# Kernel tuning notes

Hardware: AMD Instinct MI355X
Metric: run time of the kernel (lower is better)

Reference implementation:

```python
import jax, jax.numpy as jnp
import numpy as np

EMBED_DIM = 2048
NUM_HEADS = 16
HEAD_DIM = EMBED_DIM // NUM_HEADS
BATCH, SEQ = 4, 4096


def setup_inputs() -> dict:
    key = jax.random.key(0)
    k1, k2, k3, k4 = jax.random.split(key, 4)
    scale = 1.0 / np.sqrt(EMBED_DIM)
    x = jax.random.normal(k1, (BATCH, SEQ, EMBED_DIM), dtype=jnp.float32)
    W_qkv = jax.random.normal(k2, (EMBED_DIM, 3 * EMBED_DIM), dtype=jnp.float32) * scale
    W_out = jax.random.normal(k3, (EMBED_DIM, EMBED_DIM), dtype=jnp.float32) * scale
    b_out = jax.random.normal(k4, (EMBED_DIM,), dtype=jnp.float32) * 0.01
    return {"x": x, "W_qkv": W_qkv, "W_out": W_out, "b_out": b_out}


def reference(x, W_qkv, W_out, b_out):
    b, s, _ = x.shape
    # qkv: (b, s, 3, h, d)
    qkv = (x @ W_qkv).reshape(b, s, 3, NUM_HEADS, HEAD_DIM)
    q, k, v = qkv[:, :, 0], qkv[:, :, 1], qkv[:, :, 2]
    # NOTE: faithful to source — scores mix HEADS per token: (b, s, h, h)
    scores = jnp.einsum('bshd,bsHd->bshH', q, k) / jnp.sqrt(jnp.float32(HEAD_DIM))
    w = jax.nn.softmax(scores, axis=-1)
    attn = jnp.einsum('bshH,bsHd->bshd', w, v).reshape(b, s, EMBED_DIM)
    return attn @ W_out + b_out
```

## Files before the change

kernel.cpp:

```cpp
#include <hip/hip_runtime.h>
#include <hip/hip_bf16.h>
#include <cstdint>


#define TOKENS 16384
#define EMB    2048
#define NQKV   6144

typedef __bf16 bf16x8_t __attribute__((ext_vector_type(8)));
typedef float  f32x4_t  __attribute__((ext_vector_type(4)));

#define GLOAD16(gsrc, ldst)                                                    \
  __builtin_amdgcn_global_load_lds(                                            \
      (const __attribute__((address_space(1))) void*)(uintptr_t)(gsrc),        \
      (__attribute__((address_space(3))) void*)(uint32_t)(uintptr_t)(ldst),    \
      16, 0, 0)

static __device__ __forceinline__ unsigned short f32_to_bf16_bits(float f) {
  union { float f; uint32_t u; } x; x.f = f;
  uint32_t u = x.u;
  u += 0x7fffu + ((u >> 16) & 1u);
  return (unsigned short)(u >> 16);
}

__global__ __launch_bounds__(256) void cvt_f32_bf16(
    const float4* __restrict__ in, ushort4* __restrict__ out, int n4) {
  const int stride = gridDim.x * blockDim.x;
  for (int i = blockIdx.x * blockDim.x + threadIdx.x; i < n4; i += stride) {
    float4 v = in[i];
    ushort4 o;
    o.x = f32_to_bf16_bits(v.x);
    o.y = f32_to_bf16_bits(v.y);
    o.z = f32_to_bf16_bits(v.z);
    o.w = f32_to_bf16_bits(v.w);
    out[i] = o;
  }
}

__global__ __launch_bounds__(256) void transpose_cvt(
    const float* __restrict__ in, unsigned short* __restrict__ out, int R, int C) {
  __shared__ float tile[32][33];
  const int bx = blockIdx.x * 32;
  const int by = blockIdx.y * 32;
  const int tx = threadIdx.x;
  const int ty = threadIdx.y;
#pragma unroll
  for (int j = 0; j < 32; j += 8)
    tile[ty + j][tx] = in[(size_t)(by + ty + j) * C + bx + tx];
  __syncthreads();
#pragma unroll
  for (int j = 0; j < 32; j += 8)
    out[(size_t)(bx + ty + j) * R + by + tx] = f32_to_bf16_bits(tile[tx][ty + j]);
}

template <bool OUT_BF16>
__global__ __launch_bounds__(512, 1) void gemm_bt(
    const unsigned short* __restrict__ A,
    const unsigned short* __restrict__ BT,
    unsigned short* __restrict__ Cb,
    float* __restrict__ Cf,
    const float* __restrict__ bias,
    int M, int N) {
  constexpr int K = 2048;
  constexpr int BK = 64;
  constexpr int NKT = K / BK;
  __shared__ __align__(16) char lds[131072];

  const int nbx = N / 256;
  const int nwg = gridDim.x;
  const int bid = blockIdx.x;
  const int swzb = (bid & 7) * (nwg >> 3) + (bid >> 3);
  const int by = swzb / nbx;
  const int bx = swzb % nbx;

  const int t    = threadIdx.x;
  const int lane = t & 63;
  const int wid  = t >> 6;
  const int wr   = wid >> 2;
  const int wc   = wid & 3;
  const int lr   = lane & 15;
  const int g    = lane >> 4;

  const unsigned short* aSrc = A  + (size_t)by * 256 * K;
  const unsigned short* bSrc = BT + (size_t)bx * 256 * K;

  int aoff[2], boff[2];
#pragma unroll
  for (int i = 0; i < 2; ++i) {
    const int p   = (i * 512 + t) * 16;
    const int lo  = p ^ (((p >> 7) & 7) << 4);
    const int rih = lo >> 7;
    const int kbe = (lo & 127) >> 1;
    aoff[i] = (((rih >> 6) << 7) + (rih & 63)) * K + kbe;
    boff[i] = (((rih >> 5) << 6) + (rih & 31)) * K + kbe;
  }
  const int ldst = wid << 10;

  auto stageA = [&](int h, int k0, char* bufA) {
#pragma unroll
    for (int i = 0; i < 2; ++i)
      GLOAD16(aSrc + aoff[i] + h * (64 * K) + k0, bufA + h * 16384 + i * 8192 + ldst);
  };
  auto stageB = [&](int h, int k0, char* bufB) {
#pragma unroll
    for (int i = 0; i < 2; ++i)
      GLOAD16(bSrc + boff[i] + h * (32 * K) + k0, bufB + h * 16384 + i * 8192 + ldst);
  };

  const int sw   = (lr & 7) << 4;
  const int col0 = (g * 16) ^ sw;
  const int col1 = (64 + g * 16) ^ sw;
  const int aRow = (wr * 64 + lr) * 128;
  const int bRow = (wc * 32 + lr) * 128;

  f32x4_t acc[8][4] = {};
  bf16x8_t av[4][2];
  bf16x8_t bvA[2][2], bvB[2][2];
  bf16x8_t bv1[2][2];

#define LDA_INTO(dst, bufA_, q)                                                \
  {                                                                            \
    const char* _b = (bufA_) + (q) * 16384 + aRow;                             \
    _Pragma("unroll") for (int m2 = 0; m2 < 4; ++m2) {                         \
      dst[m2][0] = *(const bf16x8_t*)(_b + m2 * 2048 + col0);                  \
      dst[m2][1] = *(const bf16x8_t*)(_b + m2 * 2048 + col1);                  \
    }                                                                          \
  }
#define LDB_INTO(dst, bufB_, pair)                                             \
  {                                                                            \
    _Pragma("unroll") for (int e = 0; e < 2; ++e) {                            \
      const int nf = (pair) * 2 + e;                                           \
      const char* _b = (bufB_) + (nf >> 1) * 16384 + (nf & 1) * 2048 + bRow;   \
      dst[e][0] = *(const bf16x8_t*)(_b + col0);                               \
      dst[e][1] = *(const bf16x8_t*)(_b + col1);                               \
    }                                                                          \
  }
#define MFMAQ(AV, BV, Q, PAIR)                                                 \
  _Pragma("unroll") for (int m2 = 0; m2 < 4; ++m2)                             \
  _Pragma("unroll") for (int e = 0; e < 2; ++e)                                \
  _Pragma("unroll") for (int ks = 0; ks < 2; ++ks)                             \
    acc[(Q) * 4 + m2][(PAIR) * 2 + e] = __builtin_amdgcn_mfma_f32_16x16x32_bf16( \
        AV[m2][ks], BV[e][ks], acc[(Q) * 4 + m2][(PAIR) * 2 + e], 0, 0, 0);

#define SBR __builtin_amdgcn_sched_barrier(0)
#define BARR __builtin_amdgcn_s_barrier()
#define LGKM0 asm volatile("s_waitcnt lgkmcnt(0)" ::: "memory"); SBR;
#define P1_ __builtin_amdgcn_s_setprio(1);
#define P0_ __builtin_amdgcn_s_setprio(0); SBR;

#define BODY(KT, BVC, BVN, S1, S2, VMN)                                        \
  {                                                                            \
    char* cA = lds + ((KT) & 1) * 65536;                                       \
    char* cB = cA + 32768;                                                     \
    char* nB = lds + (((KT) + 1) & 1) * 65536 + 32768;                         \
    const int k1 = ((KT) + 1) * BK, k2 = ((KT) + 2) * BK;                      \
                  \
    LDA_INTO(av, cA, 0); SBR;                                                  \
    if (S1) { stageB(0, k1, nB); } SBR;                                        \
    BARR; LGKM0; P1_;                                                          \
    MFMAQ(av, BVC, 0, 0);                                                      \
    P0_; BARR;                                                                 \
          \
    LDB_INTO(bv1, cB, 1); SBR;                                                 \
    if (S2) { stageA(0, k2, cA); } SBR;                                        \
    BARR; LGKM0; P1_;                                                          \
    MFMAQ(av, bv1, 0, 1);                                                      \
    P0_; BARR;                                                                 \
           \
    LDA_INTO(av, cA, 1); SBR;                                                  \
    if (S2) { stageB(1, k2, cB); } SBR;                                        \
    BARR; LGKM0; P1_;                                                          \
    MFMAQ(av, bv1, 1, 1);                                                      \
    P0_; BARR;                                                                 \
                     \
    if (S2) { stageA(1, k2, cA); } SBR;                                        \
    asm volatile("s_waitcnt vmcnt(" #VMN ")" ::: "memory"); SBR;               \
    BARR;                                                                      \
    if (S1) { LDB_INTO(BVN, nB, 0); } SBR;                                     \
    P1_;                                                                       \
    MFMAQ(av, BVC, 1, 0);                                                      \
    P0_; BARR;                                                                 \
  }

  {
    char* b0A = lds;
    char* b0B = lds + 32768;
    char* b1A = lds + 65536;
    char* b1B = b1A + 32768;
    stageA(0, 0, b0A); stageA(1, 0, b0A);
    stageB(0, 0, b0B); stageB(1, 0, b0B);
    stageA(0, BK, b1A);
    stageB(1, BK, b1B);
    stageA(1, BK, b1A);
    asm volatile("s_waitcnt vmcnt(6)" ::: "memory");
    BARR;
    LDB_INTO(bvA, b0B, 0);
    SBR;
  }

  for (int kt = 0; kt < NKT - 2; kt += 2) {
    BODY(kt,     bvA, bvB, 1, 1, 6);
    BODY(kt + 1, bvB, bvA, 1, 1, 6);
  }
  BODY(NKT - 2, bvA, bvB, 1, 0, 0);
  BODY(NKT - 1, bvB, bvA, 0, 0, 0);

  const int rbase = by * 256 + wr * 128 + g * 4;
  const int cbase = bx * 256 + wc * 64 + lr;
#pragma unroll
  for (int m = 0; m < 8; ++m) {
#pragma unroll
    for (int nf = 0; nf < 4; ++nf) {
      const int col = cbase + nf * 16;
#pragma unroll
      for (int j = 0; j < 4; ++j) {
        const size_t off = (size_t)(rbase + (m >> 2) * 64 + (m & 3) * 16 + j) * N + col;
        if constexpr (OUT_BF16) {
          Cb[off] = f32_to_bf16_bits(acc[m][nf][j]);
        } else {
          Cf[off] = acc[m][nf][j] + bias[col];
        }
      }
    }
  }
#undef LDA_INTO
#undef LDB_INTO
#undef MFMAQ
#undef SBR
#undef BARR
#undef LGKM0
#undef P1_
#undef P0_
#undef BODY
}

__global__ __launch_bounds__(256) void attn_heads(
    const unsigned short* __restrict__ qkv,
    unsigned short* __restrict__ attn) {
  __shared__ __align__(16) unsigned short sQKV[NQKV];
  __shared__ float sW[16][16];

  const int t = threadIdx.x;
  const size_t qbase = (size_t)blockIdx.x * NQKV;

  const uint4* gp = (const uint4*)(qkv + qbase);
  uint4* l = (uint4*)sQKV;
#pragma unroll
  for (int i = 0; i < 3; ++i) {
    const int idx = i * 256 + t;
    int dst = idx;
    if (idx >= 256 && idx < 512) {
      const int r = (idx - 256) >> 4;
      const int c = idx & 15;
      dst = 256 + r * 16 + (c ^ (r & 7));
    }
    l[dst] = gp[idx];
  }
  __syncthreads();

  const int h = t >> 4;
  const int H = t & 15;
  const bf16x8_t* q8 = (const bf16x8_t*)sQKV + h * 16;
  const bf16x8_t* k8 = (const bf16x8_t*)sQKV + 256;
  float s = 0.f;
#pragma unroll
  for (int d8 = 0; d8 < 16; ++d8) {
    bf16x8_t qv = q8[d8];
    bf16x8_t kv = k8[H * 16 + (d8 ^ (H & 7))];
#pragma unroll
    for (int j = 0; j < 8; ++j)
      s = fmaf((float)qv[j], (float)kv[j], s);
  }
  s *= 0.08838834764831843f;

  float mx = s;
#pragma unroll
  for (int o = 8; o; o >>= 1) mx = fmaxf(mx, __shfl_xor(mx, o));
  const float e = __expf(s - mx);
  float sum = e;
#pragma unroll
  for (int o = 8; o; o >>= 1) sum += __shfl_xor(sum, o);
  sW[h][H] = e / sum;
  __syncthreads();

  const int d0c = t & 15;
  const bf16x8_t* v8 = (const bf16x8_t*)sQKV + 512;
  float accv[8] = {};
#pragma unroll
  for (int j = 0; j < 16; ++j) {
    const float w = sW[h][j];
    const bf16x8_t vv = v8[j * 16 + d0c];
#pragma unroll
    for (int jj = 0; jj < 8; ++jj)
      accv[jj] = fmaf(w, (float)vv[jj], accv[jj]);
  }
  bf16x8_t o;
#pragma unroll
  for (int jj = 0; jj < 8; ++jj) o[jj] = (__bf16)accv[jj];
  *(bf16x8_t*)(attn + (size_t)blockIdx.x * EMB + h * 128 + d0c * 8) = o;
}

extern "C" void kernel_launch(void* const* d_in, const int* in_sizes, int n_in,
                              void* d_out, int out_size, void* d_ws, size_t ws_size,
                              hipStream_t stream) {
  const float* x    = (const float*)d_in[0];
  const float* Wqkv = (const float*)d_in[1];
  const float* Wout = (const float*)d_in[2];
  const float* bout = (const float*)d_in[3];
  float* out = (float*)d_out;

  unsigned short* xb    = (unsigned short*)d_ws;
  unsigned short* wqkvT = xb    + (size_t)33554432;
  unsigned short* woutT = wqkvT + (size_t)12582912;
  unsigned short* qkv   = woutT + (size_t)4194304;
  unsigned short* attn  = qkv   + (size_t)100663296;

  cvt_f32_bf16<<<2048, 256, 0, stream>>>((const float4*)x, (ushort4*)xb, 33554432 / 4);
  transpose_cvt<<<dim3(6144 / 32, 2048 / 32), dim3(32, 8), 0, stream>>>(Wqkv, wqkvT, 2048, 6144);
  transpose_cvt<<<dim3(2048 / 32, 2048 / 32), dim3(32, 8), 0, stream>>>(Wout, woutT, 2048, 2048);
  gemm_bt<true><<<(16384 / 256) * (6144 / 256), 512, 0, stream>>>(
      xb, wqkvT, qkv, nullptr, nullptr, 16384, 6144);
  attn_heads<<<TOKENS, 256, 0, stream>>>(qkv, attn);
  gemm_bt<false><<<(16384 / 256) * (2048 / 256), 512, 0, stream>>>(
      attn, woutT, nullptr, out, bout, 16384, 2048);
}
```

Before: 612.6 us.

## Merge prep kernels into one launch and split LDS waits in GEMM

The three preprocessing kernels (the bf16 conversion of x and the transpose-converts of both weights) become one kernel, dispatched by block index, to save two launches and their tails. In the GEMM main loop, each full lgkmcnt(0) wait before an MFMA group becomes a partial wait. The first half of the MFMAs can then start while the remaining LDS reads are still in flight. This depends on the LDS loads completing in issue order, as the lgkmcnt counts assume.

```diff
diff --git a/kernel.cpp b/kernel.cpp
--- a/kernel.cpp
+++ b/kernel.cpp
@@ -23,27 +23,43 @@
   return (unsigned short)(u >> 16);
 }
 
-__global__ __launch_bounds__(256) void cvt_f32_bf16(
-    const float4* __restrict__ in, ushort4* __restrict__ out, int n4) {
-  const int stride = gridDim.x * blockDim.x;
-  for (int i = blockIdx.x * blockDim.x + threadIdx.x; i < n4; i += stride) {
-    float4 v = in[i];
-    ushort4 o;
-    o.x = f32_to_bf16_bits(v.x);
-    o.y = f32_to_bf16_bits(v.y);
-    o.z = f32_to_bf16_bits(v.z);
-    o.w = f32_to_bf16_bits(v.w);
-    out[i] = o;
-  }
-}
-
-__global__ __launch_bounds__(256) void transpose_cvt(
-    const float* __restrict__ in, unsigned short* __restrict__ out, int R, int C) {
+__global__ __launch_bounds__(256) void prep(
+    const float4* __restrict__ x4, ushort4* __restrict__ xb4,
+    const float* __restrict__ Wqkv, unsigned short* __restrict__ wqkvT,
+    const float* __restrict__ Wout, unsigned short* __restrict__ woutT) {
+  const int b = blockIdx.x;
+  const int t = threadIdx.x;
+  if (b < 2048) {
+    const int n4 = 33554432 / 4;
+    const int stride = 2048 * 256;
+    for (int i = b * 256 + t; i < n4; i += stride) {
+      float4 v = x4[i];
+      ushort4 o;
+      o.x = f32_to_bf16_bits(v.x);
+      o.y = f32_to_bf16_bits(v.y);
+      o.z = f32_to_bf16_bits(v.z);
+      o.w = f32_to_bf16_bits(v.w);
+      xb4[i] = o;
+    }
+    return;
+  }
   __shared__ float tile[32][33];
-  const int bx = blockIdx.x * 32;
-  const int by = blockIdx.y * 32;
-  const int tx = threadIdx.x;
-  const int ty = threadIdx.y;
+  const float* in;
+  unsigned short* out;
+  int R, C, bxt, byt;
+  if (b < 14336) {
+    const int bb = b - 2048;
+    in = Wqkv; out = wqkvT; R = 2048; C = 6144;
+    bxt = bb % 192; byt = bb / 192;
+  } else {
+    const int bb = b - 14336;
+    in = Wout; out = woutT; R = 2048; C = 2048;
+    bxt = bb % 64; byt = bb / 64;
+  }
+  const int bx = bxt * 32;
+  const int by = byt * 32;
+  const int tx = t & 31;
+  const int ty = t >> 5;
 #pragma unroll
   for (int j = 0; j < 32; j += 8)
     tile[ty + j][tx] = in[(size_t)(by + ty + j) * C + bx + tx];
@@ -141,10 +157,21 @@
   _Pragma("unroll") for (int ks = 0; ks < 2; ++ks)                             \
     acc[(Q) * 4 + m2][(PAIR) * 2 + e] = __builtin_amdgcn_mfma_f32_16x16x32_bf16( \
         AV[m2][ks], BV[e][ks], acc[(Q) * 4 + m2][(PAIR) * 2 + e], 0, 0, 0);
+#define MFMAQ_M(AV, BV, Q, PAIR, M0)                                           \
+  _Pragma("unroll") for (int m2 = (M0); m2 < (M0) + 2; ++m2)                   \
+  _Pragma("unroll") for (int e = 0; e < 2; ++e)                                \
+  _Pragma("unroll") for (int ks = 0; ks < 2; ++ks)                             \
+    acc[(Q) * 4 + m2][(PAIR) * 2 + e] = __builtin_amdgcn_mfma_f32_16x16x32_bf16( \
+        AV[m2][ks], BV[e][ks], acc[(Q) * 4 + m2][(PAIR) * 2 + e], 0, 0, 0);
+#define MFMAQ_E(AV, BV, Q, PAIR, E)                                            \
+  _Pragma("unroll") for (int m2 = 0; m2 < 4; ++m2)                             \
+  _Pragma("unroll") for (int ks = 0; ks < 2; ++ks)                             \
+    acc[(Q) * 4 + m2][(PAIR) * 2 + (E)] = __builtin_amdgcn_mfma_f32_16x16x32_bf16( \
+        AV[m2][ks], BV[(E)][ks], acc[(Q) * 4 + m2][(PAIR) * 2 + (E)], 0, 0, 0);
 
 #define SBR __builtin_amdgcn_sched_barrier(0)
 #define BARR __builtin_amdgcn_s_barrier()
-#define LGKM0 asm volatile("s_waitcnt lgkmcnt(0)" ::: "memory"); SBR;
+#define LGKM(NN) asm volatile("s_waitcnt lgkmcnt(" #NN ")" ::: "memory"); SBR;
 #define P1_ __builtin_amdgcn_s_setprio(1);
 #define P0_ __builtin_amdgcn_s_setprio(0); SBR;
 
@@ -154,25 +181,31 @@
     char* cB = cA + 32768;                                                     \
     char* nB = lds + (((KT) + 1) & 1) * 65536 + 32768;                         \
     const int k1 = ((KT) + 1) * BK, k2 = ((KT) + 2) * BK;                      \
-                  \
+                                 \
     LDA_INTO(av, cA, 0); SBR;                                                  \
     if (S1) { stageB(0, k1, nB); } SBR;                                        \
-    BARR; LGKM0; P1_;                                                          \
-    MFMAQ(av, BVC, 0, 0);                                                      \
+    BARR; LGKM(4); P1_;                                                        \
+    MFMAQ_M(av, BVC, 0, 0, 0);                                                 \
+    LGKM(0);                                                                   \
+    MFMAQ_M(av, BVC, 0, 0, 2);                                                 \
     P0_; BARR;                                                                 \
-          \
+                                                                   \
     LDB_INTO(bv1, cB, 1); SBR;                                                 \
     if (S2) { stageA(0, k2, cA); } SBR;                                        \
-    BARR; LGKM0; P1_;                                                          \
-    MFMAQ(av, bv1, 0, 1);                                                      \
+    BARR; LGKM(2); P1_;                                                        \
+    MFMAQ_E(av, bv1, 0, 1, 0);                                                 \
+    LGKM(0);                                                                   \
+    MFMAQ_E(av, bv1, 0, 1, 1);                                                 \
     P0_; BARR;                                                                 \
-           \
+                  \
     LDA_INTO(av, cA, 1); SBR;                                                  \
     if (S2) { stageB(1, k2, cB); } SBR;                                        \
-    BARR; LGKM0; P1_;                                                          \
-    MFMAQ(av, bv1, 1, 1);                                                      \
+    BARR; LGKM(4); P1_;                                                        \
+    MFMAQ_M(av, bv1, 1, 1, 0);                                                 \
+    LGKM(0);                                                                   \
+    MFMAQ_M(av, bv1, 1, 1, 2);                                                 \
     P0_; BARR;                                                                 \
-                     \
+         \
     if (S2) { stageA(1, k2, cA); } SBR;                                        \
     asm volatile("s_waitcnt vmcnt(" #VMN ")" ::: "memory"); SBR;               \
     BARR;                                                                      \
@@ -226,9 +259,11 @@
 #undef LDA_INTO
 #undef LDB_INTO
 #undef MFMAQ
+#undef MFMAQ_M
+#undef MFMAQ_E
 #undef SBR
 #undef BARR
-#undef LGKM0
+#undef LGKM
 #undef P1_
 #undef P0_
 #undef BODY
@@ -315,9 +350,8 @@
   unsigned short* qkv   = woutT + (size_t)4194304;
   unsigned short* attn  = qkv   + (size_t)100663296;
 
-  cvt_f32_bf16<<<2048, 256, 0, stream>>>((const float4*)x, (ushort4*)xb, 33554432 / 4);
-  transpose_cvt<<<dim3(6144 / 32, 2048 / 32), dim3(32, 8), 0, stream>>>(Wqkv, wqkvT, 2048, 6144);
-  transpose_cvt<<<dim3(2048 / 32, 2048 / 32), dim3(32, 8), 0, stream>>>(Wout, woutT, 2048, 2048);
+  prep<<<18432, 256, 0, stream>>>((const float4*)x, (ushort4*)xb,
+                                  Wqkv, wqkvT, Wout, woutT);
   gemm_bt<true><<<(16384 / 256) * (6144 / 256), 512, 0, stream>>>(
       xb, wqkvT, qkv, nullptr, nullptr, 16384, 6144);
   attn_heads<<<TOKENS, 256, 0, stream>>>(qkv, attn);
```

New measurement: 609.9 us. Within noise of the previous version (-0.4%).
